# Performance work log

Measured on AMD Instinct MI355X. Metric: run time of the kernel, lower is better.

Reference implementation:

```python
import jax, jax.numpy as jnp
import numpy as np

B, C, N, K_NN = 16, 64, 2048, 3
OUT_C = 64


def setup_inputs() -> dict:
    key = jax.random.key(0)
    k1, k2, k3 = jax.random.split(key, 3)
    x = jax.random.normal(k1, (B, C, N), dtype=jnp.float32)
    fan_in = C * K_NN
    bound = 1.0 / np.sqrt(fan_in)
    W = jax.random.uniform(k2, (OUT_C, C, K_NN), minval=-bound, maxval=bound, dtype=jnp.float32)
    b = jax.random.uniform(k3, (OUT_C,), minval=-bound, maxval=bound, dtype=jnp.float32)
    return {"x": x, "W": W, "b": b}


def reference(x, W, b):
    # x: [B, C, N]; W: [O, C, K]; b: [O]
    K = W.shape[-1]
    # Pairwise squared distances: dist[b,i,j] = |x_i|^2 + |x_j|^2 - 2 x_i.x_j.
    # The original takes sqrt, but sqrt is monotone and the distances are only
    # used for top-k index selection, so we select on squared distances (same indices).
    norm_sq = jnp.sum(x * x, axis=1)                      # [B, N]
    dot = jnp.einsum('bcn,bcm->bnm', x, x)                # [B, N, N]
    dist_sq = norm_sq[:, :, None] + norm_sq[:, None, :] - 2.0 * dot  # [B, N, N]
    # K smallest distances per row -> neighbor indices [B, N, K]
    _, idx = jax.lax.top_k(-dist_sq, K)
    # Gather neighbors: neigh[b, c, n, k] = x[b, c, idx[b, n, k]]
    neigh = jax.vmap(lambda xb, ib: xb[:, ib])(x, idx)    # [B, C, N, K]
    # Conv1d with kernel_size == stride == K over the flattened [B, C, N*K]
    # tensor is exactly a per-window contraction over the K neighbors.
    out = jnp.einsum('bcnk,ock->bon', neigh, W) + b[None, :, None]  # [B, O, N]
    return out
```

## Files before the change

### kernel.cpp

```cpp
#include <hip/hip_runtime.h>
#include <cfloat>
#include <climits>

#define B_DIM 16
#define C_DIM 64
#define N_DIM 2048
#define O_DIM 64
#define K_NN  3

typedef __attribute__((ext_vector_type(8))) short bf16x8;
typedef __attribute__((ext_vector_type(4))) float floatx4;

__device__ __forceinline__ unsigned short f32_to_bf16_rne(float f) {
  unsigned int u = __float_as_uint(f);
  return (unsigned short)((u + 0x7fffu + ((u >> 16) & 1u)) >> 16);
}
__device__ __forceinline__ float bf16_to_f32(unsigned short h) {
  return __uint_as_float(((unsigned int)h) << 16);
}

__device__ __forceinline__ void ins4(float key, int jv, float* k, int* j) {
  bool c3 = key < k[3], c2 = key < k[2], c1 = key < k[1], c0 = key < k[0];
  k[3] = c2 ? k[2] : (c3 ? key : k[3]);
  j[3] = c2 ? j[2] : (c3 ? jv  : j[3]);
  k[2] = c1 ? k[1] : (c2 ? key : k[2]);
  j[2] = c1 ? j[1] : (c2 ? jv  : j[2]);
  k[1] = c0 ? k[0] : (c1 ? key : k[1]);
  j[1] = c0 ? j[0] : (c1 ? jv  : j[1]);
  k[0] = c0 ? key : k[0];
  j[0] = c0 ? jv  : j[0];
}

__global__ __launch_bounds__(256) void prep_kernel(
    const float* __restrict__ x, float* __restrict__ xT,
    unsigned short* __restrict__ xTh, unsigned short* __restrict__ xTl,
    double* __restrict__ nd, float* __restrict__ nf,
    const float* __restrict__ W, float* __restrict__ Wt) {
  int bid = blockIdx.x;
  int t = threadIdx.x;
  if (bid >= 512) {
    int t2 = (bid - 512) * 256 + t;
    int o  = t2 / (C_DIM * K_NN);
    int ck = t2 - o * (C_DIM * K_NN);
    Wt[ck * O_DIM + o] = W[t2];
    return;
  }
  __shared__ __align__(16) float xs[C_DIM][68];
  int b  = bid >> 5;
  int n0 = (bid & 31) * 64;
  const float* xb = x + (size_t)b * C_DIM * N_DIM;
  #pragma unroll
  for (int r = 0; r < 4; ++r) {
    int idx = r * 256 + t;
    int c = idx >> 4;
    int qq = idx & 15;
    *(float4*)&xs[c][qq * 4] = *(const float4*)(xb + (size_t)c * N_DIM + n0 + qq * 4);
  }
  __syncthreads();
  int n = t >> 2, cg = t & 3;
  float v[16];
  #pragma unroll
  for (int cc = 0; cc < 16; ++cc) v[cc] = xs[cg * 16 + cc][n];
  double ps = 0.0;
  #pragma unroll
  for (int cc = 0; cc < 16; ++cc) ps = fma((double)v[cc], (double)v[cc], ps);
  ps += __shfl_xor(ps, 1, 64);
  ps += __shfl_xor(ps, 2, 64);
  size_t row = (size_t)b * N_DIM + n0 + n;
  #pragma unroll
  for (int qq = 0; qq < 4; ++qq) {
    float4 wv; wv.x = v[qq*4]; wv.y = v[qq*4+1]; wv.z = v[qq*4+2]; wv.w = v[qq*4+3];
    *(float4*)&xT[row * C_DIM + cg * 16 + qq * 4] = wv;
  }
  unsigned short hh[16], ll[16];
  #pragma unroll
  for (int cc = 0; cc < 16; ++cc) {
    hh[cc] = f32_to_bf16_rne(v[cc]);
    ll[cc] = f32_to_bf16_rne(v[cc] - bf16_to_f32(hh[cc]));
  }
  #pragma unroll
  for (int e = 0; e < 2; ++e) {
    int phys = (2 * cg + e) ^ (n & 7);
    unsigned int hp[4], lp[4];
    #pragma unroll
    for (int xk = 0; xk < 4; ++xk) {
      hp[xk] = (unsigned)hh[e*8 + 2*xk] | ((unsigned)hh[e*8 + 2*xk + 1] << 16);
      lp[xk] = (unsigned)ll[e*8 + 2*xk] | ((unsigned)ll[e*8 + 2*xk + 1] << 16);
    }
    ((uint4*)xTh)[row * 8 + phys] = *(uint4*)hp;
    ((uint4*)xTl)[row * 8 + phys] = *(uint4*)lp;
  }
  if (cg == 0) {
    nd[row] = ps;
    nf[row] = (float)ps;
  }
}

__global__ __launch_bounds__(256, 5) void topk_kernel(
    const unsigned short* __restrict__ xTh, const unsigned short* __restrict__ xTl,
    const float* __restrict__ nf, int* __restrict__ cand) {
  __shared__ __align__(16) unsigned short Jh[128 * 64];
  __shared__ __align__(16) unsigned short Jl[128 * 64];
  int bid   = blockIdx.x;
  int q     = bid & 3;
  int itile = (bid >> 2) & 31;
  int b     = bid >> 7;
  int i0    = itile * 64;
  int jq0   = q * 512;
  int t = threadIdx.x;
  int w = t >> 6, lane = t & 63, quad = lane >> 4, col = lane & 15;
  int csw = col & 7;
  const unsigned short* xh = xTh + (size_t)b * N_DIM * 64;
  const unsigned short* xl = xTl + (size_t)b * N_DIM * 64;
  const float* nfb = nf + b * N_DIM;

  bf16x8 ih[2], il[2];
  #pragma unroll
  for (int ks = 0; ks < 2; ++ks) {
    size_t row = i0 + w * 16 + col;
    int phys = (ks * 4 + quad) ^ csw;
    ih[ks] = *(const bf16x8*)(xh + row * 64 + phys * 8);
    il[ks] = *(const bf16x8*)(xl + row * 64 + phys * 8);
  }

  float ck[4]; int cj[4];
  #pragma unroll
  for (int s = 0; s < 4; ++s) { ck[s] = FLT_MAX; cj[s] = 0; }

  int a0 = col * 64 + ((quad ^ csw) * 8);
  int a1 = col * 64 + (((4 + quad) ^ csw) * 8);

  for (int js = 0; js < 4; ++js) {
    int j0 = jq0 + js * 128;
    __syncthreads();
    {
      const unsigned short* sh = xh + (size_t)(j0 + w * 32) * 64;
      const unsigned short* sl = xl + (size_t)(j0 + w * 32) * 64;
      unsigned short* dh = &Jh[w * 32 * 64];
      unsigned short* dl = &Jl[w * 32 * 64];
      int off = lane * 8;
      #pragma unroll
      for (int k2 = 0; k2 < 4; ++k2) {
        *(uint4*)(dh + k2 * 512 + off) = *(const uint4*)(sh + k2 * 512 + off);
        *(uint4*)(dl + k2 * 512 + off) = *(const uint4*)(sl + k2 * 512 + off);
      }
    }
    __syncthreads();

    floatx4 acc[8];
    #pragma unroll
    for (int jt = 0; jt < 8; ++jt) acc[jt] = (floatx4){0.f, 0.f, 0.f, 0.f};

    #pragma unroll
    for (int ks = 0; ks < 2; ++ks) {
      int ab = ks ? a1 : a0;
      #pragma unroll
      for (int jt = 0; jt < 8; ++jt) {
        bf16x8 jh = *(const bf16x8*)&Jh[jt * 1024 + ab];
        bf16x8 jl = *(const bf16x8*)&Jl[jt * 1024 + ab];
        acc[jt] = __builtin_amdgcn_mfma_f32_16x16x32_bf16(jl, ih[ks], acc[jt], 0, 0, 0);
        acc[jt] = __builtin_amdgcn_mfma_f32_16x16x32_bf16(jh, il[ks], acc[jt], 0, 0, 0);
        acc[jt] = __builtin_amdgcn_mfma_f32_16x16x32_bf16(jh, ih[ks], acc[jt], 0, 0, 0);
      }
    }

    int jb = j0 + quad * 4;
    #pragma unroll
    for (int jt = 0; jt < 8; ++jt) {
      float4 nv = *(const float4*)(nfb + jb + jt * 16);
      float nfa[4] = {nv.x, nv.y, nv.z, nv.w};
      #pragma unroll
      for (int r = 0; r < 4; ++r) {
        float key = fmaf(-2.0f, acc[jt][r], nfa[r]);
        int jv = jb + jt * 16 + r;
        ins4(key, jv, ck, cj);
      }
    }
  }

  #pragma unroll
  for (int m = 16; m < 64; m <<= 1) {
    float tk[4]; int tj[4];
    #pragma unroll
    for (int s = 0; s < 4; ++s) {
      tk[s] = __shfl_xor(ck[s], m, 64);
      tj[s] = __shfl_xor(cj[s], m, 64);
    }
    #pragma unroll
    for (int s = 0; s < 4; ++s) ins4(tk[s], tj[s], ck, cj);
  }
  if (quad == 0) {
    int row = b * N_DIM + i0 + w * 16 + col;
    int base = row * 16 + q * 4;
    #pragma unroll
    for (int s = 0; s < 4; ++s) cand[base + s] = cj[s];
  }
}

__global__ __launch_bounds__(256) void refine_kernel(
    const float* __restrict__ xT, const double* __restrict__ nd,
    const int* __restrict__ cand, int* __restrict__ topk) {
  int t = threadIdx.x;
  int lane = t & 63;
  int row = blockIdx.x * 4 + (t >> 6);
  int b = row >> 11;
  int n = row & (N_DIM - 1);
  int cid = lane >> 2;
  int seg = lane & 3;
  int j = cand[row * 16 + cid];
  const float* xn = xT + (((size_t)b * N_DIM + n) * C_DIM) + seg * 16;
  const float* xj = xT + (((size_t)b * N_DIM + j) * C_DIM) + seg * 16;
  double dot = 0.0;
  #pragma unroll
  for (int qq = 0; qq < 4; ++qq) {
    float4 a  = *(const float4*)(xn + qq * 4);
    float4 bb = *(const float4*)(xj + qq * 4);
    dot = fma((double)a.x, (double)bb.x, dot);
    dot = fma((double)a.y, (double)bb.y, dot);
    dot = fma((double)a.z, (double)bb.z, dot);
    dot = fma((double)a.w, (double)bb.w, dot);
  }
  dot += __shfl_xor(dot, 1, 64);
  dot += __shfl_xor(dot, 2, 64);
  double key = fma(-2.0, dot, nd[b * N_DIM + j] + nd[b * N_DIM + n]) + 1.0;
  unsigned long long u =
      ((unsigned long long)__double_as_longlong(key) & ~2047ull) |
      (unsigned long long)(unsigned)j;
  unsigned long long v = u;
  int jout[3];
  #pragma unroll
  for (int p = 0; p < 3; ++p) {
    unsigned long long m = v;
    #pragma unroll
    for (int msk = 4; msk < 64; msk <<= 1) {
      unsigned long long o = __shfl_xor(m, msk, 64);
      m = (o < m) ? o : m;
    }
    jout[p] = (int)(m & 2047ull);
    v = (v == m) ? ~0ull : v;
  }
  if (lane == 0) {
    int base = row * K_NN;
    topk[base + 0] = jout[0];
    topk[base + 1] = jout[1];
    topk[base + 2] = jout[2];
  }
}

#define NT   64
#define NPAD 68
__global__ __launch_bounds__(256) void conv_kernel(
    const float* __restrict__ xT, const float* __restrict__ Wt,
    const float* __restrict__ bias, const int* __restrict__ topk,
    float* __restrict__ out) {
  __shared__ __align__(16) float nb[C_DIM * K_NN][NPAD];
  int bid = blockIdx.x;
  int b  = bid >> 5;
  int n0 = (bid & 31) * NT;
  const float* xtb = xT + (size_t)b * N_DIM * C_DIM;
  const int* tk = topk + (b * N_DIM + n0) * K_NN;
  int t = threadIdx.x;

  #pragma unroll
  for (int p = 0; p < 12; ++p) {
    int u = p * 256 + t;
    int seg = u & 15;
    int r   = u >> 4;
    int k = r >> 6, n = r & 63;
    int j = tk[n * K_NN + k];
    float4 v = *(const float4*)(xtb + (size_t)j * C_DIM + seg * 4);
    nb[(seg * 4 + 0) * 3 + k][n] = v.x;
    nb[(seg * 4 + 1) * 3 + k][n] = v.y;
    nb[(seg * 4 + 2) * 3 + k][n] = v.z;
    nb[(seg * 4 + 3) * 3 + k][n] = v.w;
  }
  __syncthreads();

  int ng = t & 15, og = t >> 4;
  float acc[4][4];
  #pragma unroll
  for (int oo = 0; oo < 4; ++oo) {
    float bv = bias[(og << 2) + oo];
    #pragma unroll
    for (int nn = 0; nn < 4; ++nn) acc[oo][nn] = bv;
  }
  const float* nbp = &nb[0][0] + (ng << 2);
  const float* wtp = Wt + (og << 2);
  #pragma unroll 4
  for (int ckk = 0; ckk < C_DIM * K_NN; ++ckk) {
    float4 nv = *(const float4*)(nbp + ckk * NPAD);
    float4 wv = *(const float4*)(wtp + ckk * O_DIM);
    float na[4] = {nv.x, nv.y, nv.z, nv.w};
    float wa[4] = {wv.x, wv.y, wv.z, wv.w};
    #pragma unroll
    for (int oo = 0; oo < 4; ++oo)
      #pragma unroll
      for (int nn = 0; nn < 4; ++nn)
        acc[oo][nn] = fmaf(wa[oo], na[nn], acc[oo][nn]);
  }
  #pragma unroll
  for (int oo = 0; oo < 4; ++oo) {
    int o = (og << 2) + oo;
    float4 v; v.x = acc[oo][0]; v.y = acc[oo][1]; v.z = acc[oo][2]; v.w = acc[oo][3];
    *(float4*)&out[(size_t)(b * O_DIM + o) * N_DIM + n0 + (ng << 2)] = v;
  }
}

extern "C" void kernel_launch(void* const* d_in, const int* in_sizes, int n_in,
                              void* d_out, int out_size, void* d_ws, size_t ws_size,
                              hipStream_t stream) {
  const float* x    = (const float*)d_in[0];
  const float* W    = (const float*)d_in[1];
  const float* bias = (const float*)d_in[2];
  float* out = (float*)d_out;
  char* ws = (char*)d_ws;
  float*          xT  = (float*)ws;
  unsigned short* xTh = (unsigned short*)(ws + 8388608);
  unsigned short* xTl = (unsigned short*)(ws + 12582912);
  double*         nd  = (double*)(ws + 16777216);
  float*          nfp = (float*)(ws + 17039360);
  int*            cd  = (int*)(ws + 17170432);
  int*            tk  = (int*)(ws + 19267584);
  float*          Wt  = (float*)(ws + 19660800);

  prep_kernel<<<512 + 48, 256, 0, stream>>>(x, xT, xTh, xTl, nd, nfp, W, Wt);
  topk_kernel<<<B_DIM * 32 * 4, 256, 0, stream>>>(xTh, xTl, nfp, cd);
  refine_kernel<<<(B_DIM * N_DIM) / 4, 256, 0, stream>>>(xT, nd, cd, tk);
  conv_kernel<<<B_DIM * (N_DIM / NT), 256, 0, stream>>>(xT, Wt, bias, tk, out);
}
```

Measured before the change: 169.9 us.

## Split bf16 hi/lo on the fly in topk, shrink candidate list and index types

```diff
diff --git a/kernel.cpp b/kernel.cpp
--- a/kernel.cpp
+++ b/kernel.cpp
@@ -19,10 +19,8 @@
   return __uint_as_float(((unsigned int)h) << 16);
 }
 
-__device__ __forceinline__ void ins4(float key, int jv, float* k, int* j) {
-  bool c3 = key < k[3], c2 = key < k[2], c1 = key < k[1], c0 = key < k[0];
-  k[3] = c2 ? k[2] : (c3 ? key : k[3]);
-  j[3] = c2 ? j[2] : (c3 ? jv  : j[3]);
+__device__ __forceinline__ void ins3(float key, int jv, float* k, int* j) {
+  bool c2 = key < k[2], c1 = key < k[1], c0 = key < k[0];
   k[2] = c1 ? k[1] : (c2 ? key : k[2]);
   j[2] = c1 ? j[1] : (c2 ? jv  : j[2]);
   k[1] = c0 ? k[0] : (c1 ? key : k[1]);
@@ -31,10 +29,20 @@
   j[0] = c0 ? jv  : j[0];
 }
 
+__device__ __forceinline__ void split8(const float* v, bf16x8* h8, bf16x8* l8) {
+  unsigned short h[8], l[8];
+  #pragma unroll
+  for (int e = 0; e < 8; ++e) {
+    h[e] = f32_to_bf16_rne(v[e]);
+    l[e] = f32_to_bf16_rne(v[e] - bf16_to_f32(h[e]));
+  }
+  *h8 = *(bf16x8*)h;
+  *l8 = *(bf16x8*)l;
+}
+
 __global__ __launch_bounds__(256) void prep_kernel(
     const float* __restrict__ x, float* __restrict__ xT,
-    unsigned short* __restrict__ xTh, unsigned short* __restrict__ xTl,
-    double* __restrict__ nd, float* __restrict__ nf,
+    float* __restrict__ nf,
     const float* __restrict__ W, float* __restrict__ Wt) {
   int bid = blockIdx.x;
   int t = threadIdx.x;
@@ -72,33 +80,12 @@
     float4 wv; wv.x = v[qq*4]; wv.y = v[qq*4+1]; wv.z = v[qq*4+2]; wv.w = v[qq*4+3];
     *(float4*)&xT[row * C_DIM + cg * 16 + qq * 4] = wv;
   }
-  unsigned short hh[16], ll[16];
-  #pragma unroll
-  for (int cc = 0; cc < 16; ++cc) {
-    hh[cc] = f32_to_bf16_rne(v[cc]);
-    ll[cc] = f32_to_bf16_rne(v[cc] - bf16_to_f32(hh[cc]));
-  }
-  #pragma unroll
-  for (int e = 0; e < 2; ++e) {
-    int phys = (2 * cg + e) ^ (n & 7);
-    unsigned int hp[4], lp[4];
-    #pragma unroll
-    for (int xk = 0; xk < 4; ++xk) {
-      hp[xk] = (unsigned)hh[e*8 + 2*xk] | ((unsigned)hh[e*8 + 2*xk + 1] << 16);
-      lp[xk] = (unsigned)ll[e*8 + 2*xk] | ((unsigned)ll[e*8 + 2*xk + 1] << 16);
-    }
-    ((uint4*)xTh)[row * 8 + phys] = *(uint4*)hp;
-    ((uint4*)xTl)[row * 8 + phys] = *(uint4*)lp;
-  }
-  if (cg == 0) {
-    nd[row] = ps;
-    nf[row] = (float)ps;
-  }
-}
-
-__global__ __launch_bounds__(256, 5) void topk_kernel(
-    const unsigned short* __restrict__ xTh, const unsigned short* __restrict__ xTl,
-    const float* __restrict__ nf, int* __restrict__ cand) {
+  if (cg == 0) nf[row] = (float)ps;
+}
+
+__global__ __launch_bounds__(256, 4) void topk_kernel(
+    const float* __restrict__ xT, const float* __restrict__ nf,
+    unsigned short* __restrict__ cand) {
   __shared__ __align__(16) unsigned short Jh[128 * 64];
   __shared__ __align__(16) unsigned short Jl[128 * 64];
   int bid   = blockIdx.x;
@@ -110,22 +97,24 @@
   int t = threadIdx.x;
   int w = t >> 6, lane = t & 63, quad = lane >> 4, col = lane & 15;
   int csw = col & 7;
-  const unsigned short* xh = xTh + (size_t)b * N_DIM * 64;
-  const unsigned short* xl = xTl + (size_t)b * N_DIM * 64;
+  const float* xb  = xT + (size_t)b * N_DIM * C_DIM;
   const float* nfb = nf + b * N_DIM;
 
   bf16x8 ih[2], il[2];
-  #pragma unroll
-  for (int ks = 0; ks < 2; ++ks) {
-    size_t row = i0 + w * 16 + col;
-    int phys = (ks * 4 + quad) ^ csw;
-    ih[ks] = *(const bf16x8*)(xh + row * 64 + phys * 8);
-    il[ks] = *(const bf16x8*)(xl + row * 64 + phys * 8);
-  }
-
-  float ck[4]; int cj[4];
-  #pragma unroll
-  for (int s = 0; s < 4; ++s) { ck[s] = FLT_MAX; cj[s] = 0; }
+  {
+    const float* ip = xb + (size_t)(i0 + w * 16 + col) * C_DIM + quad * 8;
+    #pragma unroll
+    for (int ks = 0; ks < 2; ++ks) {
+      float v[8];
+      *(float4*)&v[0] = *(const float4*)(ip + ks * 32);
+      *(float4*)&v[4] = *(const float4*)(ip + ks * 32 + 4);
+      split8(v, &ih[ks], &il[ks]);
+    }
+  }
+
+  float ck[3]; int cj[3];
+  ck[0] = ck[1] = ck[2] = FLT_MAX;
+  cj[0] = cj[1] = cj[2] = 0;
 
   int a0 = col * 64 + ((quad ^ csw) * 8);
   int a1 = col * 64 + (((4 + quad) ^ csw) * 8);
@@ -134,15 +123,22 @@
     int j0 = jq0 + js * 128;
     __syncthreads();
     {
-      const unsigned short* sh = xh + (size_t)(j0 + w * 32) * 64;
-      const unsigned short* sl = xl + (size_t)(j0 + w * 32) * 64;
-      unsigned short* dh = &Jh[w * 32 * 64];
-      unsigned short* dl = &Jl[w * 32 * 64];
-      int off = lane * 8;
+      int rr = lane >> 1, half = lane & 1;
+      int lrow = w * 32 + rr;
+      const float* src = xb + (size_t)(j0 + lrow) * C_DIM + half * 32;
+      unsigned short* dh = &Jh[lrow * 64];
+      unsigned short* dl = &Jl[lrow * 64];
+      int sw = lrow & 7;
       #pragma unroll
-      for (int k2 = 0; k2 < 4; ++k2) {
-        *(uint4*)(dh + k2 * 512 + off) = *(const uint4*)(sh + k2 * 512 + off);
-        *(uint4*)(dl + k2 * 512 + off) = *(const uint4*)(sl + k2 * 512 + off);
+      for (int g = 0; g < 4; ++g) {
+        float v[8];
+        *(float4*)&v[0] = *(const float4*)(src + g * 8);
+        *(float4*)&v[4] = *(const float4*)(src + g * 8 + 4);
+        bf16x8 h8, l8;
+        split8(v, &h8, &l8);
+        int phys = ((half * 4 + g) ^ sw) * 8;
+        *(bf16x8*)(dh + phys) = h8;
+        *(bf16x8*)(dl + phys) = l8;
       }
     }
     __syncthreads();
@@ -172,34 +168,35 @@
       #pragma unroll
       for (int r = 0; r < 4; ++r) {
         float key = fmaf(-2.0f, acc[jt][r], nfa[r]);
-        int jv = jb + jt * 16 + r;
-        ins4(key, jv, ck, cj);
+        ins3(key, jb + jt * 16 + r, ck, cj);
       }
     }
   }
 
   #pragma unroll
   for (int m = 16; m < 64; m <<= 1) {
-    float tk[4]; int tj[4];
-    #pragma unroll
-    for (int s = 0; s < 4; ++s) {
+    float tk[3]; int tj[3];
+    #pragma unroll
+    for (int s = 0; s < 3; ++s) {
       tk[s] = __shfl_xor(ck[s], m, 64);
       tj[s] = __shfl_xor(cj[s], m, 64);
     }
     #pragma unroll
-    for (int s = 0; s < 4; ++s) ins4(tk[s], tj[s], ck, cj);
+    for (int s = 0; s < 3; ++s) ins3(tk[s], tj[s], ck, cj);
   }
   if (quad == 0) {
     int row = b * N_DIM + i0 + w * 16 + col;
-    int base = row * 16 + q * 4;
-    #pragma unroll
-    for (int s = 0; s < 4; ++s) cand[base + s] = cj[s];
+    unsigned short* cp = cand + row * 16 + q * 4;
+    cp[0] = (unsigned short)cj[0];
+    cp[1] = (unsigned short)cj[1];
+    cp[2] = (unsigned short)cj[2];
+    cp[3] = (unsigned short)cj[0];
   }
 }
 
 __global__ __launch_bounds__(256) void refine_kernel(
-    const float* __restrict__ xT, const double* __restrict__ nd,
-    const int* __restrict__ cand, int* __restrict__ topk) {
+    const float* __restrict__ xT, const unsigned short* __restrict__ cand,
+    unsigned short* __restrict__ topk) {
   int t = threadIdx.x;
   int lane = t & 63;
   int row = blockIdx.x * 4 + (t >> 6);
@@ -210,19 +207,24 @@
   int j = cand[row * 16 + cid];
   const float* xn = xT + (((size_t)b * N_DIM + n) * C_DIM) + seg * 16;
   const float* xj = xT + (((size_t)b * N_DIM + j) * C_DIM) + seg * 16;
-  double dot = 0.0;
+  double pd = 0.0, pn = 0.0, pj = 0.0;
   #pragma unroll
   for (int qq = 0; qq < 4; ++qq) {
     float4 a  = *(const float4*)(xn + qq * 4);
     float4 bb = *(const float4*)(xj + qq * 4);
-    dot = fma((double)a.x, (double)bb.x, dot);
-    dot = fma((double)a.y, (double)bb.y, dot);
-    dot = fma((double)a.z, (double)bb.z, dot);
-    dot = fma((double)a.w, (double)bb.w, dot);
-  }
-  dot += __shfl_xor(dot, 1, 64);
-  dot += __shfl_xor(dot, 2, 64);
-  double key = fma(-2.0, dot, nd[b * N_DIM + j] + nd[b * N_DIM + n]) + 1.0;
+    double ax = a.x,  ay = a.y,  az = a.z,  aw = a.w;
+    double bx = bb.x, by = bb.y, bz = bb.z, bw = bb.w;
+    pd = fma(ax, bx, pd); pd = fma(ay, by, pd);
+    pd = fma(az, bz, pd); pd = fma(aw, bw, pd);
+    pn = fma(ax, ax, pn); pn = fma(ay, ay, pn);
+    pn = fma(az, az, pn); pn = fma(aw, aw, pn);
+    pj = fma(bx, bx, pj); pj = fma(by, by, pj);
+    pj = fma(bz, bz, pj); pj = fma(bw, bw, pj);
+  }
+  pd += __shfl_xor(pd, 1, 64); pd += __shfl_xor(pd, 2, 64);
+  pn += __shfl_xor(pn, 1, 64); pn += __shfl_xor(pn, 2, 64);
+  pj += __shfl_xor(pj, 1, 64); pj += __shfl_xor(pj, 2, 64);
+  double key = (pn + pj - 2.0 * pd) + 1.0;
   unsigned long long u =
       ((unsigned long long)__double_as_longlong(key) & ~2047ull) |
       (unsigned long long)(unsigned)j;
@@ -240,10 +242,10 @@
     v = (v == m) ? ~0ull : v;
   }
   if (lane == 0) {
-    int base = row * K_NN;
-    topk[base + 0] = jout[0];
-    topk[base + 1] = jout[1];
-    topk[base + 2] = jout[2];
+    unsigned short* tp = topk + row * K_NN;
+    tp[0] = (unsigned short)jout[0];
+    tp[1] = (unsigned short)jout[1];
+    tp[2] = (unsigned short)jout[2];
   }
 }
 
@@ -251,14 +253,14 @@
 #define NPAD 68
 __global__ __launch_bounds__(256) void conv_kernel(
     const float* __restrict__ xT, const float* __restrict__ Wt,
-    const float* __restrict__ bias, const int* __restrict__ topk,
+    const float* __restrict__ bias, const unsigned short* __restrict__ topk,
     float* __restrict__ out) {
   __shared__ __align__(16) float nb[C_DIM * K_NN][NPAD];
   int bid = blockIdx.x;
   int b  = bid >> 5;
   int n0 = (bid & 31) * NT;
   const float* xtb = xT + (size_t)b * N_DIM * C_DIM;
-  const int* tk = topk + (b * N_DIM + n0) * K_NN;
+  const unsigned short* tk = topk + (b * N_DIM + n0) * K_NN;
   int t = threadIdx.x;
 
   #pragma unroll
@@ -315,16 +317,13 @@
   float* out = (float*)d_out;
   char* ws = (char*)d_ws;
   float*          xT  = (float*)ws;
-  unsigned short* xTh = (unsigned short*)(ws + 8388608);
-  unsigned short* xTl = (unsigned short*)(ws + 12582912);
-  double*         nd  = (double*)(ws + 16777216);
-  float*          nfp = (float*)(ws + 17039360);
-  int*            cd  = (int*)(ws + 17170432);
-  int*            tk  = (int*)(ws + 19267584);
-  float*          Wt  = (float*)(ws + 19660800);
-
-  prep_kernel<<<512 + 48, 256, 0, stream>>>(x, xT, xTh, xTl, nd, nfp, W, Wt);
-  topk_kernel<<<B_DIM * 32 * 4, 256, 0, stream>>>(xTh, xTl, nfp, cd);
-  refine_kernel<<<(B_DIM * N_DIM) / 4, 256, 0, stream>>>(xT, nd, cd, tk);
+  float*          nfp = (float*)(ws + 8388608);
+  unsigned short* cd  = (unsigned short*)(ws + 8519680);
+  unsigned short* tk  = (unsigned short*)(ws + 9568256);
+  float*          Wt  = (float*)(ws + 9764864);
+
+  prep_kernel<<<512 + 48, 256, 0, stream>>>(x, xT, nfp, W, Wt);
+  topk_kernel<<<B_DIM * 32 * 4, 256, 0, stream>>>(xT, nfp, cd);
+  refine_kernel<<<(B_DIM * N_DIM) / 4, 256, 0, stream>>>(xT, cd, tk);
   conv_kernel<<<B_DIM * (N_DIM / NT), 256, 0, stream>>>(xT, Wt, bias, tk, out);
 }
```

Result: no change. 170.0 us (+0.1%).

## Pack distance key and local index into one uint for med3 top-4 insertion

Applied to the files above, without the earlier changes.

```diff
diff --git a/kernel.cpp b/kernel.cpp
--- a/kernel.cpp
+++ b/kernel.cpp
@@ -19,16 +19,21 @@
   return __uint_as_float(((unsigned int)h) << 16);
 }
 
-__device__ __forceinline__ void ins4(float key, int jv, float* k, int* j) {
-  bool c3 = key < k[3], c2 = key < k[2], c1 = key < k[1], c0 = key < k[0];
-  k[3] = c2 ? k[2] : (c3 ? key : k[3]);
-  j[3] = c2 ? j[2] : (c3 ? jv  : j[3]);
-  k[2] = c1 ? k[1] : (c2 ? key : k[2]);
-  j[2] = c1 ? j[1] : (c2 ? jv  : j[2]);
-  k[1] = c0 ? k[0] : (c1 ? key : k[1]);
-  j[1] = c0 ? j[0] : (c1 ? jv  : j[1]);
-  k[0] = c0 ? key : k[0];
-  j[0] = c0 ? jv  : j[0];
+__device__ __forceinline__ unsigned med3u(unsigned a, unsigned b, unsigned c) {
+  unsigned mn = min(a, b), mx = max(a, b);
+  return max(mn, min(mx, c));
+}
+
+__device__ __forceinline__ void ins4p(unsigned u, int jv, unsigned* k, int* j) {
+  bool c3 = u < k[3], c2 = u < k[2], c1 = u < k[1], c0 = u < k[0];
+  k[3] = c2 ? k[2] : (c3 ? u  : k[3]);
+  j[3] = c2 ? j[2] : (c3 ? jv : j[3]);
+  k[2] = c1 ? k[1] : (c2 ? u  : k[2]);
+  j[2] = c1 ? j[1] : (c2 ? jv : j[2]);
+  k[1] = c0 ? k[0] : (c1 ? u  : k[1]);
+  j[1] = c0 ? j[0] : (c1 ? jv : j[1]);
+  k[0] = c0 ? u  : k[0];
+  j[0] = c0 ? jv : j[0];
 }
 
 __global__ __launch_bounds__(256) void prep_kernel(
@@ -92,19 +97,19 @@
   }
   if (cg == 0) {
     nd[row] = ps;
-    nf[row] = (float)ps;
-  }
-}
-
-__global__ __launch_bounds__(256, 5) void topk_kernel(
+    nf[row] = (float)ps + 512.0f;
+  }
+}
+
+__global__ __launch_bounds__(256, 4) void topk_kernel(
     const unsigned short* __restrict__ xTh, const unsigned short* __restrict__ xTl,
-    const float* __restrict__ nf, int* __restrict__ cand) {
+    const float* __restrict__ nf, unsigned short* __restrict__ cand, int b_base) {
   __shared__ __align__(16) unsigned short Jh[128 * 64];
   __shared__ __align__(16) unsigned short Jl[128 * 64];
   int bid   = blockIdx.x;
   int q     = bid & 3;
   int itile = (bid >> 2) & 31;
-  int b     = bid >> 7;
+  int b     = b_base + (bid >> 7);
   int i0    = itile * 64;
   int jq0   = q * 512;
   int t = threadIdx.x;
@@ -123,9 +128,8 @@
     il[ks] = *(const bf16x8*)(xl + row * 64 + phys * 8);
   }
 
-  float ck[4]; int cj[4];
-  #pragma unroll
-  for (int s = 0; s < 4; ++s) { ck[s] = FLT_MAX; cj[s] = 0; }
+  unsigned ck[4];
+  ck[0] = ck[1] = ck[2] = ck[3] = 0xFFFFFFFFu;
 
   int a0 = col * 64 + ((quad ^ csw) * 8);
   int a1 = col * 64 + (((4 + quad) ^ csw) * 8);
@@ -164,6 +168,7 @@
       }
     }
 
+    unsigned locb = (unsigned)(js << 5);
     int jb = j0 + quad * 4;
     #pragma unroll
     for (int jt = 0; jt < 8; ++jt) {
@@ -172,34 +177,48 @@
       #pragma unroll
       for (int r = 0; r < 4; ++r) {
         float key = fmaf(-2.0f, acc[jt][r], nfa[r]);
-        int jv = jb + jt * 16 + r;
-        ins4(key, jv, ck, cj);
+        unsigned u = (__float_as_uint(key) & 0xFFFFFF80u) | locb |
+                     (unsigned)(jt * 4 + r);
+        unsigned m0 = min(ck[0], u);
+        unsigned m1 = med3u(ck[0], u, ck[1]);
+        unsigned m2 = med3u(ck[1], u, ck[2]);
+        unsigned m3 = med3u(ck[2], u, ck[3]);
+        ck[0] = m0; ck[1] = m1; ck[2] = m2; ck[3] = m3;
       }
     }
   }
 
+  int cj[4];
+  #pragma unroll
+  for (int s = 0; s < 4; ++s) {
+    unsigned loc = ck[s] & 127u;
+    cj[s] = jq0 + (int)((loc >> 5) << 7) + (int)(((loc >> 2) & 7u) << 4) +
+            (quad << 2) + (int)(loc & 3u);
+  }
   #pragma unroll
   for (int m = 16; m < 64; m <<= 1) {
-    float tk[4]; int tj[4];
+    unsigned tu[4]; int tj[4];
     #pragma unroll
     for (int s = 0; s < 4; ++s) {
-      tk[s] = __shfl_xor(ck[s], m, 64);
+      tu[s] = __shfl_xor(ck[s], m, 64);
       tj[s] = __shfl_xor(cj[s], m, 64);
     }
     #pragma unroll
-    for (int s = 0; s < 4; ++s) ins4(tk[s], tj[s], ck, cj);
+    for (int s = 0; s < 4; ++s) ins4p(tu[s], tj[s], ck, cj);
   }
   if (quad == 0) {
     int row = b * N_DIM + i0 + w * 16 + col;
-    int base = row * 16 + q * 4;
-    #pragma unroll
-    for (int s = 0; s < 4; ++s) cand[base + s] = cj[s];
+    unsigned short* cp = cand + row * 16 + q * 4;
+    cp[0] = (unsigned short)cj[0];
+    cp[1] = (unsigned short)cj[1];
+    cp[2] = (unsigned short)cj[2];
+    cp[3] = (unsigned short)cj[3];
   }
 }
 
 __global__ __launch_bounds__(256) void refine_kernel(
     const float* __restrict__ xT, const double* __restrict__ nd,
-    const int* __restrict__ cand, int* __restrict__ topk) {
+    const unsigned short* __restrict__ cand, unsigned short* __restrict__ topk) {
   int t = threadIdx.x;
   int lane = t & 63;
   int row = blockIdx.x * 4 + (t >> 6);
@@ -210,19 +229,19 @@
   int j = cand[row * 16 + cid];
   const float* xn = xT + (((size_t)b * N_DIM + n) * C_DIM) + seg * 16;
   const float* xj = xT + (((size_t)b * N_DIM + j) * C_DIM) + seg * 16;
-  double dot = 0.0;
+  double pd = 0.0;
   #pragma unroll
   for (int qq = 0; qq < 4; ++qq) {
     float4 a  = *(const float4*)(xn + qq * 4);
     float4 bb = *(const float4*)(xj + qq * 4);
-    dot = fma((double)a.x, (double)bb.x, dot);
-    dot = fma((double)a.y, (double)bb.y, dot);
-    dot = fma((double)a.z, (double)bb.z, dot);
-    dot = fma((double)a.w, (double)bb.w, dot);
-  }
-  dot += __shfl_xor(dot, 1, 64);
-  dot += __shfl_xor(dot, 2, 64);
-  double key = fma(-2.0, dot, nd[b * N_DIM + j] + nd[b * N_DIM + n]) + 1.0;
+    pd = fma((double)a.x, (double)bb.x, pd);
+    pd = fma((double)a.y, (double)bb.y, pd);
+    pd = fma((double)a.z, (double)bb.z, pd);
+    pd = fma((double)a.w, (double)bb.w, pd);
+  }
+  pd += __shfl_xor(pd, 1, 64);
+  pd += __shfl_xor(pd, 2, 64);
+  double key = fma(-2.0, pd, nd[b * N_DIM + j] + 512.0);
   unsigned long long u =
       ((unsigned long long)__double_as_longlong(key) & ~2047ull) |
       (unsigned long long)(unsigned)j;
@@ -240,10 +259,10 @@
     v = (v == m) ? ~0ull : v;
   }
   if (lane == 0) {
-    int base = row * K_NN;
-    topk[base + 0] = jout[0];
-    topk[base + 1] = jout[1];
-    topk[base + 2] = jout[2];
+    unsigned short* tp = topk + row * K_NN;
+    tp[0] = (unsigned short)jout[0];
+    tp[1] = (unsigned short)jout[1];
+    tp[2] = (unsigned short)jout[2];
   }
 }
 
@@ -251,14 +270,14 @@
 #define NPAD 68
 __global__ __launch_bounds__(256) void conv_kernel(
     const float* __restrict__ xT, const float* __restrict__ Wt,
-    const float* __restrict__ bias, const int* __restrict__ topk,
+    const float* __restrict__ bias, const unsigned short* __restrict__ topk,
     float* __restrict__ out) {
   __shared__ __align__(16) float nb[C_DIM * K_NN][NPAD];
   int bid = blockIdx.x;
   int b  = bid >> 5;
   int n0 = (bid & 31) * NT;
   const float* xtb = xT + (size_t)b * N_DIM * C_DIM;
-  const int* tk = topk + (b * N_DIM + n0) * K_NN;
+  const unsigned short* tk = topk + (b * N_DIM + n0) * K_NN;
   int t = threadIdx.x;
 
   #pragma unroll
@@ -319,12 +338,13 @@
   unsigned short* xTl = (unsigned short*)(ws + 12582912);
   double*         nd  = (double*)(ws + 16777216);
   float*          nfp = (float*)(ws + 17039360);
-  int*            cd  = (int*)(ws + 17170432);
-  int*            tk  = (int*)(ws + 19267584);
-  float*          Wt  = (float*)(ws + 19660800);
+  unsigned short* cd  = (unsigned short*)(ws + 17170432);
+  unsigned short* tk  = (unsigned short*)(ws + 18219008);
+  float*          Wt  = (float*)(ws + 18415616);
 
   prep_kernel<<<512 + 48, 256, 0, stream>>>(x, xT, xTh, xTl, nd, nfp, W, Wt);
-  topk_kernel<<<B_DIM * 32 * 4, 256, 0, stream>>>(xTh, xTl, nfp, cd);
+  topk_kernel<<<8 * 32 * 4, 256, 0, stream>>>(xTh, xTl, nfp, cd, 0);
+  topk_kernel<<<8 * 32 * 4, 256, 0, stream>>>(xTh, xTl, nfp, cd, 8);
   refine_kernel<<<(B_DIM * N_DIM) / 4, 256, 0, stream>>>(xT, nd, cd, tk);
   conv_kernel<<<B_DIM * (N_DIM / NT), 256, 0, stream>>>(xT, Wt, bias, tk, out);
 }
```

New measurement: 162.6 us. 1.04x faster.
